# Kernel optimization log

Measured on AMD Instinct MI355X. Metric: run time of the kernel, lower is better.

The kernel has to match this reference:

```python
import jax, jax.numpy as jnp
import numpy as np

N = 100000   # nodes
E = 1600000  # edges
IN, HID, OUT = 128, 128, 64


def setup_inputs() -> dict:
    key = jax.random.key(0)
    ks = jax.random.split(key, 8)
    x = jax.random.normal(ks[0], (N, IN), dtype=jnp.float32)
    edge_index = jax.random.randint(ks[1], (2, E), 0, N, dtype=jnp.int64)
    W1 = jax.random.normal(ks[2], (IN, HID), dtype=jnp.float32) * 0.05
    b1 = jnp.zeros((HID,), dtype=jnp.float32)
    W2 = jax.random.normal(ks[3], (HID, OUT), dtype=jnp.float32) * 0.05
    b2 = jnp.zeros((OUT,), dtype=jnp.float32)
    Wd = jax.random.normal(ks[4], (OUT, IN), dtype=jnp.float32) * 0.05
    bd = jnp.zeros((IN,), dtype=jnp.float32)
    return {"x": x, "edge_index": edge_index, "W1": W1, "b1": b1,
            "W2": W2, "b2": b2, "Wd": Wd, "bd": bd}


def _gcn_conv(x, src, dst, W, b):
    # PyG GCNConv: add self-loops, symmetric normalization D^-1/2 (A+I) D^-1/2,
    # messages flow src -> dst, aggregated by sum at dst.
    h = x @ W                                   # [N, F]
    ones = jnp.ones((src.shape[0],), x.dtype)
    deg = jax.ops.segment_sum(ones, dst, num_segments=N) + 1.0  # +1 for self-loop
    dinv = jax.lax.rsqrt(deg)                   # deg^-1/2, [N]
    coef = dinv[src] * dinv[dst]                # per-edge norm
    agg = jax.ops.segment_sum(h[src] * coef[:, None], dst, num_segments=N)
    agg = agg + h * (dinv * dinv)[:, None]      # self-loop contribution
    return agg + b


def reference(x, edge_index, W1, b1, W2, b2, Wd, bd):
    src, dst = edge_index[0], edge_index[1]
    h = jax.nn.relu(_gcn_conv(x, src, dst, W1, b1))
    # dropout in eval mode -> identity
    z = _gcn_conv(h, src, dst, W2, b2)          # [N, OUT] embedding
    x_recon = z @ Wd + bd                        # [N, IN]
    return (x_recon, z)
```

## Files before the change

kernel.cpp:

```cpp
#include <hip/hip_runtime.h>
#include <hip/hip_bf16.h>
#include <hip/hip_fp16.h>


#define TPB 256
#define CAP 64
#define BINCAP 220000
#define FILLW 112

typedef float v2f __attribute__((ext_vector_type(2)));


__device__ __forceinline__ unsigned short f2bf(float f) {
    unsigned u = __float_as_uint(f);
    unsigned r = u + 0x7fffu + ((u >> 16) & 1u);
    return (unsigned short)(r >> 16);
}
__device__ __forceinline__ float bf_lo(unsigned u) { return __uint_as_float(u << 16); }
__device__ __forceinline__ float bf_hi(unsigned u) { return __uint_as_float(u & 0xffff0000u); }


template <int K, int C, int TN, bool BIAS, bool INBF, bool OUTBF>
__device__ __forceinline__ void gemm_body(const void* __restrict__ Ap,
                                          const float* __restrict__ W,
                                          const float* __restrict__ bias,
                                          void* __restrict__ outp, int N, int bid,
                                          float* __restrict__ Ws) {
    constexpr int BM  = 128;
    constexpr int TM  = 8;
    constexpr int BK  = 32;
    constexpr int NCT = C / TN;
    static_assert(NCT * (BM / TM) == TPB, "thread layout");

    int tid = threadIdx.x;
    int tc = tid % NCT;
    int tr = tid / NCT;
    int c0 = tc * TN;
    int r0 = bid * BM + tr * TM;

    float acc[TM][TN] = {};

    for (int k0 = 0; k0 < K; k0 += BK) {
        __syncthreads();
        for (int i = tid * 4; i < BK * C; i += TPB * 4)
            *(float4*)&Ws[i] = *(const float4*)&W[k0 * C + i];
        __syncthreads();

        for (int k = 0; k < BK; k += 4) {
            float4 a[TM];
            uint2  au[TM];
#pragma unroll
            for (int i = 0; i < TM; ++i) {
                int r = r0 + i;
                if (r >= N) r = N - 1;
                if (INBF)
                    au[i] = *(const uint2*)((const unsigned short*)Ap + (size_t)r * K + k0 + k);
                else
                    a[i] = *(const float4*)((const float*)Ap + (size_t)r * K + k0 + k);
            }
#pragma unroll
            for (int kk = 0; kk < 4; ++kk) {
                float w[TN];
#pragma unroll
                for (int j = 0; j < TN; j += 4)
                    *(float4*)&w[j] = *(const float4*)&Ws[(k + kk) * C + c0 + j];
#pragma unroll
                for (int i = 0; i < TM; ++i) {
                    float av;
                    if (INBF) {
                        unsigned uu = (kk < 2) ? au[i].x : au[i].y;
                        av = (kk & 1) ? bf_hi(uu) : bf_lo(uu);
                    } else {
                        av = ((const float*)&a[i])[kk];
                    }
#pragma unroll
                    for (int j = 0; j < TN; ++j) acc[i][j] += av * w[j];
                }
            }
        }
    }

#pragma unroll
    for (int i = 0; i < TM; ++i) {
        int r = r0 + i;
        if (r >= N) continue;
        if (BIAS) {
#pragma unroll
            for (int j = 0; j < TN; ++j) acc[i][j] += bias[c0 + j];
        }
        if (OUTBF) {
            unsigned short* ob = (unsigned short*)outp + (size_t)r * C + c0;
            unsigned pk[TN / 2];
#pragma unroll
            for (int j = 0; j < TN; j += 2)
                pk[j / 2] = (unsigned)f2bf(acc[i][j]) | ((unsigned)f2bf(acc[i][j + 1]) << 16);
            if (TN == 8)      *(uint4*)ob = *(uint4*)pk;
            else if (TN == 4) *(uint2*)ob = *(uint2*)pk;
        } else {
            float* of = (float*)outp + (size_t)r * C + c0;
#pragma unroll
            for (int j = 0; j < TN; j += 4)
                *(float4*)&of[j] = *(float4*)&acc[i][j];
        }
    }
}


__global__ __launch_bounds__(TPB) void fused1_k(const float* __restrict__ x,
                                                const float* __restrict__ W1,
                                                unsigned* __restrict__ h1b,
                                                const int* __restrict__ src,
                                                const int* __restrict__ dst,
                                                uint2* __restrict__ binBuf,
                                                int* __restrict__ binCnt,
                                                int N, int E, int gb, unsigned M) {
    __shared__ float Ws[32 * 128];
    __shared__ int hist[8], gbase[8], lpos[8];
    if ((int)blockIdx.x < gb) {
        gemm_body<128, 128, 8, false, false, true>(x, W1, nullptr, h1b, N, blockIdx.x, Ws);
    } else {
        int bid = (int)blockIdx.x - gb;
        int tid = (int)threadIdx.x;
        if (tid < 8) { hist[tid] = 0; lpos[tid] = 0; }
        __syncthreads();

        int e0 = (bid * TPB + tid) * 8;
        int ne = E - e0; ne = ne > 8 ? 8 : (ne < 0 ? 0 : ne);
        int ss[8], dd[8], bb8[8];
        if (ne == 8) {
            int4 sa = *(const int4*)&src[e0];
            int4 sb = *(const int4*)&src[e0 + 4];
            int4 da = *(const int4*)&dst[e0];
            int4 db = *(const int4*)&dst[e0 + 4];
            ss[0]=sa.x; ss[1]=sa.y; ss[2]=sa.z; ss[3]=sa.w;
            ss[4]=sb.x; ss[5]=sb.y; ss[6]=sb.z; ss[7]=sb.w;
            dd[0]=da.x; dd[1]=da.y; dd[2]=da.z; dd[3]=da.w;
            dd[4]=db.x; dd[5]=db.y; dd[6]=db.z; dd[7]=db.w;
        } else {
            for (int q = 0; q < ne; ++q) { ss[q] = src[e0 + q]; dd[q] = dst[e0 + q]; }
        }
        for (int q = 0; q < ne; ++q) {
            bb8[q] = (int)(((unsigned long long)(unsigned)dd[q] * M) >> 32);
            atomicAdd(&hist[bb8[q]], 1);
        }
        __syncthreads();
        if (tid < 8) gbase[tid] = atomicAdd(&binCnt[tid], hist[tid]);
        __syncthreads();
        for (int q = 0; q < ne; ++q) {
            int b = bb8[q];
            int p = gbase[b] + atomicAdd(&lpos[b], 1);
            if (p < BINCAP)
                binBuf[(size_t)b * BINCAP + p] = make_uint2((unsigned)ss[q], (unsigned)dd[q]);
        }
    }
}


__global__ __launch_bounds__(TPB) void fill_k(const uint2* __restrict__ binBuf,
                                              const int* __restrict__ binCnt,
                                              int* __restrict__ cnt,
                                              unsigned* __restrict__ bucket, int N) {
    int bin = (int)blockIdx.x & 7;
    int w   = (int)blockIdx.x >> 3;
    int cb  = binCnt[bin];
    if (cb > BINCAP) cb = BINCAP;
    const uint2* eb = binBuf + (size_t)bin * BINCAP;

    for (int base = w * (TPB * 8); base < cb; base += FILLW * (TPB * 8)) {
        int e0 = base + (int)threadIdx.x * 8;
        if (e0 + 8 <= cb) {
            unsigned s[8], d[8];
#pragma unroll
            for (int q = 0; q < 8; q += 2) {
                uint4 t = *(const uint4*)&eb[e0 + q];
                s[q] = t.x; d[q] = t.y; s[q + 1] = t.z; d[q + 1] = t.w;
            }
            int rr[8];
#pragma unroll
            for (int q = 0; q < 8; ++q) rr[q] = atomicAdd(&cnt[(int)d[q]], 1);
#pragma unroll
            for (int q = 0; q < 8; ++q)
                if (rr[q] < CAP) bucket[(size_t)rr[q] * N + d[q]] = s[q];
        } else {
            int lim = e0 + 8 < cb ? e0 + 8 : cb;
            for (int e = e0; e < lim; ++e) {
                uint2 t = eb[e];
                int r = atomicAdd(&cnt[(int)t.y], 1);
                if (r < CAP) bucket[(size_t)r * N + t.y] = t.x;
            }
        }
    }
}


__global__ __launch_bounds__(TPB) void dinv_k(const int* __restrict__ cnt,
                                              float* __restrict__ dinv, int N) {
    int i = blockIdx.x * TPB + (int)threadIdx.x;
    if (i < N) dinv[i] = rsqrtf((float)cnt[i] + 1.0f);
}


__global__ __launch_bounds__(TPB) void aggG1_k(const unsigned* __restrict__ h,
                                               const float* __restrict__ dinv,
                                               const int* __restrict__ cnt,
                                               const unsigned* __restrict__ bucket,
                                               const float* __restrict__ b1,
                                               const float* __restrict__ W2,
                                               unsigned* __restrict__ h2b, int N) {
    constexpr int F2 = 64, NPB = TPB / F2;
    __shared__ float zl[NPB][128];
    int tid = (int)threadIdx.x;
    int ln = tid / F2;
    int f2 = tid % F2;
    int n  = blockIdx.x * NPB + ln;

    if (n < N) {
        int cfull = cnt[n];
        float di = dinv[n];
        const unsigned* hp = h + f2;
        unsigned us = hp[(size_t)n * F2];
        v2f acc;
        acc.x = bf_lo(us) * (di * di);
        acc.y = bf_hi(us) * (di * di);

        int cn = cfull < CAP ? cfull : CAP;
        const unsigned* bp = bucket + n;

        int nfull = cn & ~7;
        int s[8], sn2[8];
        if (nfull > 0) {
#pragma unroll
            for (int q = 0; q < 8; ++q) s[q] = (int)bp[(size_t)q * N];
        }
        for (int j = 0; j < nfull; ) {
            int jn = j + 8;
            bool more = jn < nfull;
            if (more) {
#pragma unroll
                for (int q = 0; q < 8; ++q) sn2[q] = (int)bp[(size_t)(jn + q) * N];
            }
            unsigned v[8];
            float ds[8];
#pragma unroll
            for (int q = 0; q < 8; ++q) {
                v[q]  = hp[(size_t)s[q] * F2];
                ds[q] = dinv[s[q]];
            }
#pragma unroll
            for (int q = 0; q < 8; ++q) {
                float c = ds[q] * di;
                v2f hv; hv.x = bf_lo(v[q]); hv.y = bf_hi(v[q]);
                acc += hv * c;
            }
            if (more) {
#pragma unroll
                for (int q = 0; q < 8; ++q) s[q] = sn2[q];
            }
            j = jn;
        }
        for (int j = nfull; j < cn; ++j) {
            int sx = (int)bp[(size_t)j * N];
            unsigned v = hp[(size_t)sx * F2];
            float c = dinv[sx] * di;
            acc.x += c * bf_lo(v);
            acc.y += c * bf_hi(v);
        }

        float rx = fmaxf(acc.x + b1[2 * f2], 0.f);
        float ry = fmaxf(acc.y + b1[2 * f2 + 1], 0.f);
        zl[ln][2 * f2]     = rx;
        zl[ln][2 * f2 + 1] = ry;
    }
    __syncthreads();

    int dn = tid / 64;
    int c  = tid & 63;
    int nn = blockIdx.x * NPB + dn;
    if (nn < N) {
        float a = 0.f;
        const float* w = W2 + c;
#pragma unroll 8
        for (int k = 0; k < 128; ++k) a += zl[dn][k] * w[(size_t)k * 64];
        float b = __shfl_down(a, 1);
        if ((c & 1) == 0) {
            unsigned pk = (unsigned)f2bf(a) | ((unsigned)f2bf(b) << 16);
            h2b[(size_t)nn * 32 + (c >> 1)] = pk;
        }
    }
}


__global__ __launch_bounds__(TPB) void agg2g_k(const unsigned* __restrict__ h,
                                               const float* __restrict__ dinv,
                                               const int* __restrict__ cnt,
                                               const unsigned* __restrict__ bucket,
                                               const float* __restrict__ bias,
                                               const float* __restrict__ Wd,
                                               const float* __restrict__ bd,
                                               float* __restrict__ z_out,
                                               float* __restrict__ x_recon, int N) {
    constexpr int F2 = 32, NPB = TPB / F2;
    __shared__ float zl[NPB][64];
    int ln = (int)threadIdx.x / F2;
    int f2 = (int)threadIdx.x % F2;
    int n  = blockIdx.x * NPB + ln;

    if (n < N) {
        int cfull = cnt[n];
        float di = dinv[n];
        const unsigned* hp = h + f2;
        unsigned us = hp[(size_t)n * F2];
        v2f acc;
        acc.x = bf_lo(us) * (di * di);
        acc.y = bf_hi(us) * (di * di);

        int cn = cfull < CAP ? cfull : CAP;
        const unsigned* bp = bucket + n;

        int nfull = cn & ~7;
        int s[8], sn2[8];
        if (nfull > 0) {
#pragma unroll
            for (int q = 0; q < 8; ++q) s[q] = (int)bp[(size_t)q * N];
        }
        for (int j = 0; j < nfull; ) {
            int jn = j + 8;
            bool more = jn < nfull;
            if (more) {
#pragma unroll
                for (int q = 0; q < 8; ++q) sn2[q] = (int)bp[(size_t)(jn + q) * N];
            }
            unsigned v[8];
            float ds[8];
#pragma unroll
            for (int q = 0; q < 8; ++q) {
                v[q]  = hp[(size_t)s[q] * F2];
                ds[q] = dinv[s[q]];
            }
#pragma unroll
            for (int q = 0; q < 8; ++q) {
                float c = ds[q] * di;
                v2f hv; hv.x = bf_lo(v[q]); hv.y = bf_hi(v[q]);
                acc += hv * c;
            }
            if (more) {
#pragma unroll
                for (int q = 0; q < 8; ++q) s[q] = sn2[q];
            }
            j = jn;
        }
        for (int j = nfull; j < cn; ++j) {
            int sx = (int)bp[(size_t)j * N];
            unsigned v = hp[(size_t)sx * F2];
            float c = dinv[sx] * di;
            acc.x += c * bf_lo(v);
            acc.y += c * bf_hi(v);
        }

        float rx = acc.x + bias[2 * f2];
        float ry = acc.y + bias[2 * f2 + 1];
        v2f r; r.x = rx; r.y = ry;
        __builtin_nontemporal_store(r, (v2f*)z_out + (size_t)n * F2 + f2);
        *(v2f*)&zl[ln][2 * f2] = r;
    }
    __syncthreads();

    int dn = (int)threadIdx.x / 32;
    int c0 = ((int)threadIdx.x % 32) * 4;
    int nn = blockIdx.x * NPB + dn;
    if (nn < N) {
        float a0 = bd[c0], a1 = bd[c0 + 1], a2 = bd[c0 + 2], a3 = bd[c0 + 3];
#pragma unroll 4
        for (int k = 0; k < 64; ++k) {
            float zv = zl[dn][k];
            float4 w = *(const float4*)&Wd[k * 128 + c0];
            a0 += zv * w.x; a1 += zv * w.y; a2 += zv * w.z; a3 += zv * w.w;
        }
        float4 o; o.x = a0; o.y = a1; o.z = a2; o.w = a3;
        *(float4*)&x_recon[(size_t)nn * 128 + c0] = o;
    }
}


extern "C" void kernel_launch(void* const* d_in, const int* in_sizes, int n_in,
                              void* d_out, int out_size, void* d_ws, size_t ws_size,
                              hipStream_t stream) {
    const float* x    = (const float*)d_in[0];
    const int*   eidx = (const int*)d_in[1];
    const float* W1   = (const float*)d_in[2];
    const float* b1   = (const float*)d_in[3];
    const float* W2   = (const float*)d_in[4];
    const float* b2   = (const float*)d_in[5];
    const float* Wd   = (const float*)d_in[6];
    const float* bd   = (const float*)d_in[7];

    const int N = in_sizes[0] / 128;
    const int E = in_sizes[1] / 2;
    const int* src = eidx;
    const int* dst = eidx + E;

    size_t off = 0;
    auto alloc = [&](size_t bytes) {
        void* p = (char*)d_ws + off;
        off += (bytes + 255) & ~(size_t)255;
        return p;
    };
    int*      cnt     = (int*)alloc((size_t)N * 4);
    float*    dinv    = (float*)alloc((size_t)N * 4);
    unsigned* bucket  = (unsigned*)alloc((size_t)N * CAP * 4);
    unsigned* h1b     = (unsigned*)alloc((size_t)N * 64 * 4);
    unsigned* h2b     = (unsigned*)alloc((size_t)N * 32 * 4);
    uint2*    binBuf  = (uint2*)alloc((size_t)8 * BINCAP * 8);
    int*      binCnt  = (int*)alloc(256);
    (void)ws_size;

    float* x_recon = (float*)d_out;
    float* z_out   = (float*)d_out + (size_t)N * 128;

    const int gb = (N + 127) / 128;
    const int bb = (E + TPB * 8 - 1) / (TPB * 8);
    const unsigned M = (unsigned)((8ULL << 32) / (unsigned)N);

    (void)hipMemsetAsync(cnt, 0, (size_t)N * 4, stream);
    (void)hipMemsetAsync(binCnt, 0, 256, stream);

    fused1_k<<<gb + bb, TPB, 0, stream>>>(x, W1, h1b, src, dst, binBuf, binCnt, N, E, gb, M);
    fill_k<<<8 * FILLW, TPB, 0, stream>>>(binBuf, binCnt, cnt, bucket, N);
    dinv_k<<<(N + TPB - 1) / TPB, TPB, 0, stream>>>(cnt, dinv, N);

    aggG1_k<<<(N + 3) / 4, TPB, 0, stream>>>(h1b, dinv, cnt, bucket, b1, W2, h2b, N);
    agg2g_k<<<(N + 7) / 8, TPB, 0, stream>>>(h2b, dinv, cnt, bucket, b2, Wd, bd,
                                             z_out, x_recon, N);
}
```

Baseline: 538.2 us.

## Split layer-1 aggregation from W2 GEMM into separate aggregate and tiled GEMM kernels

Replaces the fused aggregate+W2 kernel with a generic aggregation kernel that writes the ReLU output in bf16, followed by a dedicated tiled GEMM kernel for the W2 projection. The old in-block dot product reloaded W2 from global memory per node with poor reuse. The tiled GEMM reuses W2 through shared memory, at the cost of an extra bf16 intermediate round-trip through memory and one more launch. The binning buffer is aliased onto the new intermediate buffer to save workspace.

```diff
diff --git a/kernel.cpp b/kernel.cpp
--- a/kernel.cpp
+++ b/kernel.cpp
@@ -103,6 +103,15 @@
                 *(float4*)&of[j] = *(float4*)&acc[i][j];
         }
     }
+}
+
+template <int K, int C, int TN, bool BIAS, bool INBF, bool OUTBF>
+__global__ __launch_bounds__(TPB) void gemm_k(const void* __restrict__ Ap,
+                                              const float* __restrict__ W,
+                                              const float* __restrict__ bias,
+                                              void* __restrict__ outp, int N) {
+    __shared__ float Ws[32 * C];
+    gemm_body<K, C, TN, BIAS, INBF, OUTBF>(Ap, W, bias, outp, N, blockIdx.x, Ws);
 }
 
 
@@ -200,92 +209,79 @@
 }
 
 
-__global__ __launch_bounds__(TPB) void aggG1_k(const unsigned* __restrict__ h,
-                                               const float* __restrict__ dinv,
-                                               const int* __restrict__ cnt,
-                                               const unsigned* __restrict__ bucket,
-                                               const float* __restrict__ b1,
-                                               const float* __restrict__ W2,
-                                               unsigned* __restrict__ h2b, int N) {
-    constexpr int F2 = 64, NPB = TPB / F2;
-    __shared__ float zl[NPB][128];
-    int tid = (int)threadIdx.x;
-    int ln = tid / F2;
-    int f2 = tid % F2;
+template <int F2, bool RELU, bool OUTBF>
+__global__ __launch_bounds__(TPB) void agg_k(const unsigned* __restrict__ h,
+                                             const float* __restrict__ dinv,
+                                             const int* __restrict__ cnt,
+                                             const unsigned* __restrict__ bucket,
+                                             const float* __restrict__ bias,
+                                             void* __restrict__ outp, int N) {
+    constexpr int NPB = TPB / F2;
+    int ln = threadIdx.x / F2;
+    int f2 = threadIdx.x % F2;
     int n  = blockIdx.x * NPB + ln;
-
-    if (n < N) {
-        int cfull = cnt[n];
-        float di = dinv[n];
-        const unsigned* hp = h + f2;
-        unsigned us = hp[(size_t)n * F2];
-        v2f acc;
-        acc.x = bf_lo(us) * (di * di);
-        acc.y = bf_hi(us) * (di * di);
-
-        int cn = cfull < CAP ? cfull : CAP;
-        const unsigned* bp = bucket + n;
-
-        int nfull = cn & ~7;
-        int s[8], sn2[8];
-        if (nfull > 0) {
-#pragma unroll
-            for (int q = 0; q < 8; ++q) s[q] = (int)bp[(size_t)q * N];
-        }
-        for (int j = 0; j < nfull; ) {
-            int jn = j + 8;
-            bool more = jn < nfull;
-            if (more) {
-#pragma unroll
-                for (int q = 0; q < 8; ++q) sn2[q] = (int)bp[(size_t)(jn + q) * N];
-            }
-            unsigned v[8];
-            float ds[8];
-#pragma unroll
-            for (int q = 0; q < 8; ++q) {
-                v[q]  = hp[(size_t)s[q] * F2];
-                ds[q] = dinv[s[q]];
-            }
-#pragma unroll
-            for (int q = 0; q < 8; ++q) {
-                float c = ds[q] * di;
-                v2f hv; hv.x = bf_lo(v[q]); hv.y = bf_hi(v[q]);
-                acc += hv * c;
-            }
-            if (more) {
-#pragma unroll
-                for (int q = 0; q < 8; ++q) s[q] = sn2[q];
-            }
-            j = jn;
-        }
-        for (int j = nfull; j < cn; ++j) {
-            int sx = (int)bp[(size_t)j * N];
-            unsigned v = hp[(size_t)sx * F2];
-            float c = dinv[sx] * di;
-            acc.x += c * bf_lo(v);
-            acc.y += c * bf_hi(v);
-        }
-
-        float rx = fmaxf(acc.x + b1[2 * f2], 0.f);
-        float ry = fmaxf(acc.y + b1[2 * f2 + 1], 0.f);
-        zl[ln][2 * f2]     = rx;
-        zl[ln][2 * f2 + 1] = ry;
-    }
-    __syncthreads();
-
-    int dn = tid / 64;
-    int c  = tid & 63;
-    int nn = blockIdx.x * NPB + dn;
-    if (nn < N) {
-        float a = 0.f;
-        const float* w = W2 + c;
-#pragma unroll 8
-        for (int k = 0; k < 128; ++k) a += zl[dn][k] * w[(size_t)k * 64];
-        float b = __shfl_down(a, 1);
-        if ((c & 1) == 0) {
-            unsigned pk = (unsigned)f2bf(a) | ((unsigned)f2bf(b) << 16);
-            h2b[(size_t)nn * 32 + (c >> 1)] = pk;
-        }
+    if (n >= N) return;
+
+    int cfull = cnt[n];
+    float di = dinv[n];
+    const unsigned* hp = h + f2;
+    unsigned us = hp[(size_t)n * F2];
+    v2f acc;
+    acc.x = bf_lo(us) * (di * di);
+    acc.y = bf_hi(us) * (di * di);
+
+    int cn = cfull < CAP ? cfull : CAP;
+    const unsigned* bp = bucket + n;
+
+    int nfull = cn & ~7;
+    int s[8], sn2[8];
+    if (nfull > 0) {
+#pragma unroll
+        for (int q = 0; q < 8; ++q) s[q] = (int)bp[(size_t)q * N];
+    }
+    for (int j = 0; j < nfull; ) {
+        int jn = j + 8;
+        bool more = jn < nfull;
+        if (more) {
+#pragma unroll
+            for (int q = 0; q < 8; ++q) sn2[q] = (int)bp[(size_t)(jn + q) * N];
+        }
+        unsigned v[8];
+        float ds[8];
+#pragma unroll
+        for (int q = 0; q < 8; ++q) {
+            v[q]  = hp[(size_t)s[q] * F2];
+            ds[q] = dinv[s[q]];
+        }
+#pragma unroll
+        for (int q = 0; q < 8; ++q) {
+            float c = ds[q] * di;
+            v2f hv; hv.x = bf_lo(v[q]); hv.y = bf_hi(v[q]);
+            acc += hv * c;
+        }
+        if (more) {
+#pragma unroll
+            for (int q = 0; q < 8; ++q) s[q] = sn2[q];
+        }
+        j = jn;
+    }
+    for (int j = nfull; j < cn; ++j) {
+        int sx = (int)bp[(size_t)j * N];
+        unsigned v = hp[(size_t)sx * F2];
+        float c = dinv[sx] * di;
+        acc.x += c * bf_lo(v);
+        acc.y += c * bf_hi(v);
+    }
+
+    float rx = acc.x + bias[2 * f2];
+    float ry = acc.y + bias[2 * f2 + 1];
+    if (RELU) { rx = fmaxf(rx, 0.f); ry = fmaxf(ry, 0.f); }
+    if (OUTBF) {
+        unsigned pk = (unsigned)f2bf(rx) | ((unsigned)f2bf(ry) << 16);
+        ((unsigned*)outp)[(size_t)n * F2 + f2] = pk;
+    } else {
+        v2f r; r.x = rx; r.y = ry;
+        __builtin_nontemporal_store(r, (v2f*)outp + (size_t)n * F2 + f2);
     }
 }
 
@@ -410,8 +406,9 @@
     unsigned* bucket  = (unsigned*)alloc((size_t)N * CAP * 4);
     unsigned* h1b     = (unsigned*)alloc((size_t)N * 64 * 4);
     unsigned* h2b     = (unsigned*)alloc((size_t)N * 32 * 4);
-    uint2*    binBuf  = (uint2*)alloc((size_t)8 * BINCAP * 8);
+    unsigned* hrelu_b = (unsigned*)alloc((size_t)N * 64 * 4);
     int*      binCnt  = (int*)alloc(256);
+    uint2*    binBuf  = (uint2*)hrelu_b;
     (void)ws_size;
 
     float* x_recon = (float*)d_out;
@@ -428,7 +425,8 @@
     fill_k<<<8 * FILLW, TPB, 0, stream>>>(binBuf, binCnt, cnt, bucket, N);
     dinv_k<<<(N + TPB - 1) / TPB, TPB, 0, stream>>>(cnt, dinv, N);
 
-    aggG1_k<<<(N + 3) / 4, TPB, 0, stream>>>(h1b, dinv, cnt, bucket, b1, W2, h2b, N);
+    agg_k<64, true, true><<<(N + 3) / 4, TPB, 0, stream>>>(h1b, dinv, cnt, bucket, b1, hrelu_b, N);
+    gemm_k<128, 64, 4, false, true, true><<<gb, TPB, 0, stream>>>(hrelu_b, W2, nullptr, h2b, N);
     agg2g_k<<<(N + 7) / 8, TPB, 0, stream>>>(h2b, dinv, cnt, bucket, b2, Wd, bd,
                                              z_out, x_recon, N);
 }
```

After: 505.9 us. 1.06x faster.
